# Kernel tuning notes

Hardware: AMD Instinct MI355X
Metric: run time of the kernel (lower is better)

Reference implementation:

```python
import jax, jax.numpy as jnp
import numpy as np

SEQ, D_IN, D_OUT = 8192, 1024, 1024

def setup_inputs() -> dict:
    key = jax.random.key(0)
    kx, kq, kk, kv = jax.random.split(key, 4)
    scale = 1.0 / np.sqrt(D_IN)
    return {
        "x": jax.random.normal(kx, (SEQ, D_IN), dtype=jnp.float32),
        "Wq": jax.random.normal(kq, (D_OUT, D_IN), dtype=jnp.float32) * scale,
        "Wk": jax.random.normal(kk, (D_OUT, D_IN), dtype=jnp.float32) * scale,
        "Wv": jax.random.normal(kv, (D_OUT, D_IN), dtype=jnp.float32) * scale,
    }

def reference(x, Wq, Wk, Wv):
    # nn.Linear: y = x @ W.T (no bias)
    q = x @ Wq.T            # [S, d_out]
    k = x @ Wk.T            # [S, d_out]
    v = x @ Wv.T            # [S, d_out]
    d_k = k.shape[-1]
    scores = (q @ k.T) / jnp.sqrt(jnp.float32(d_k))   # [S, S]
    attn = jax.nn.softmax(scores, axis=-1)
    return attn @ v         # [S, d_out]
```

## Files before the change

### kernel.cpp

```cpp
#include <hip/hip_runtime.h>

typedef unsigned short ushort_t;
typedef __attribute__((ext_vector_type(8))) __bf16 bf16x8;
typedef __attribute__((ext_vector_type(8))) unsigned short ushort8;
typedef __attribute__((ext_vector_type(4))) float f32x4;

#define SEQ 8192
#define DIN 1024
#define DOUT 1024

#define OM_BF16 0
#define OM_F32  1
#define OM_EXP  2
#define OM_NORM 3

__device__ __forceinline__ ushort_t f2bf(float f) {
  union { float f; unsigned u; } c; c.f = f;
  unsigned u = c.u;
  return (ushort_t)((u + 0x7fffu + ((u >> 16) & 1u)) >> 16);
}

__device__ __forceinline__ void async16(ushort_t* lds, const ushort_t* g) {
  __builtin_amdgcn_global_load_lds(
      (__attribute__((address_space(1))) void*)g,
      (__attribute__((address_space(3))) void*)lds, 16, 0, 0);
}

__global__ __launch_bounds__(256) void cvt_all_kernel(
    const float* __restrict__ x, const float* __restrict__ wq,
    const float* __restrict__ wk, const float* __restrict__ wv,
    ushort_t* __restrict__ xb, ushort_t* __restrict__ wqkb,
    ushort_t* __restrict__ wvb) {
  int b = blockIdx.x;
  const float* src;
  ushort_t* dst;
  int idx;
  if (b < 8192) {
    src = x; dst = xb; idx = b * 256 + threadIdx.x;
  } else {
    int r = b - 8192;
    int w = r >> 10;
    idx = (r & 1023) * 256 + threadIdx.x;
    if (w == 0)      { src = wq; dst = wqkb; }
    else if (w == 1) { src = wk; dst = wqkb + DOUT * DIN; }
    else             { src = wv; dst = wvb; }
  }
  float4 f = ((const float4*)src)[idx];
  ushort4 o;
  o.x = f2bf(f.x); o.y = f2bf(f.y); o.z = f2bf(f.z); o.w = f2bf(f.w);
  ((ushort4*)dst)[idx] = o;
}

template <int OUTMODE, int SWZ, int BK>
__global__ __launch_bounds__(256) void gemm_bt(const ushort_t* __restrict__ A,
                                               const ushort_t* __restrict__ B,
                                               void* __restrict__ C,
                                               int lda, int ldb, int ldc,
                                               int K, float scale,
                                               float* __restrict__ rsp, int nparts) {
  constexpr int CPR = BK / 8;
  __shared__ ushort_t As[128 * BK];
  __shared__ ushort_t Bs[128 * BK];
  const int t = threadIdx.x;
  const int lane = t & 63;
  const int wave = t >> 6;
  const int wr = wave >> 1, wc = wave & 1;
  const int quad = lane >> 4, r16 = lane & 15;

  int mt, nt;
  if (SWZ == 1) {
    mt = blockIdx.x * (gridDim.y >> 3) + (blockIdx.y >> 3);
    nt = blockIdx.y & 7;
  } else {
    mt = blockIdx.y;
    nt = blockIdx.x;
  }
  const int rowBase = mt * 128;
  const int colBase = nt * 128;

  f32x4 acc[4][4] = {};

  const int nk = K / BK;
  for (int kt = 0; kt < nk; ++kt) {
    #pragma unroll
    for (int i = 0; i < BK / 16; ++i) {
      int c = t + i * 256;
      int row = c / CPR;
      int kq = c & (CPR - 1);
      int kqs = (kq & ~7) | ((kq & 7) ^ (row & 7));
      async16(&As[c * 8], A + (size_t)(rowBase + row) * lda + kt * BK + kqs * 8);
      async16(&Bs[c * 8], B + (size_t)(colBase + row) * ldb + kt * BK + kqs * 8);
    }
    __syncthreads();
    #pragma unroll
    for (int ks = 0; ks < BK / 32; ++ks) {
      bf16x8 af[4], bfr[4];
      #pragma unroll
      for (int mi = 0; mi < 4; ++mi) {
        int row = wr * 64 + mi * 16 + r16;
        int kq = ks * 4 + quad;
        int c = row * CPR + ((kq & ~7) | ((kq & 7) ^ (row & 7)));
        af[mi] = *(const bf16x8*)&As[c * 8];
      }
      #pragma unroll
      for (int ni = 0; ni < 4; ++ni) {
        int row = wc * 64 + ni * 16 + r16;
        int kq = ks * 4 + quad;
        int c = row * CPR + ((kq & ~7) | ((kq & 7) ^ (row & 7)));
        bfr[ni] = *(const bf16x8*)&Bs[c * 8];
      }
      #pragma unroll
      for (int mi = 0; mi < 4; ++mi)
        #pragma unroll
        for (int ni = 0; ni < 4; ++ni)
          acc[mi][ni] = __builtin_amdgcn_mfma_f32_16x16x32_bf16(af[mi], bfr[ni],
                                                                acc[mi][ni], 0, 0, 0);
    }
    __syncthreads();
  }

  float iv[4][4];
  if (OUTMODE == OM_NORM) {
    float* invs = (float*)As;
    if (t < 128) {
      float s = 0.f;
      for (int p2 = 0; p2 < nparts; ++p2)
        s += rsp[(size_t)p2 * SEQ + rowBase + t];
      invs[t] = 1.0f / s;
    }
    __syncthreads();
    #pragma unroll
    for (int mi = 0; mi < 4; ++mi)
      #pragma unroll
      for (int r = 0; r < 4; ++r)
        iv[mi][r] = invs[wr * 64 + mi * 16 + quad * 4 + r];
  }

  float psum[4][4];
  if (OUTMODE == OM_EXP) {
    #pragma unroll
    for (int mi = 0; mi < 4; ++mi)
      #pragma unroll
      for (int r = 0; r < 4; ++r) psum[mi][r] = 0.f;
  }

  #pragma unroll
  for (int mi = 0; mi < 4; ++mi)
    #pragma unroll
    for (int ni = 0; ni < 4; ++ni)
      #pragma unroll
      for (int r = 0; r < 4; ++r) {
        int grow = rowBase + wr * 64 + mi * 16 + quad * 4 + r;
        int gcol = colBase + wc * 64 + ni * 16 + r16;
        float a = acc[mi][ni][r];
        if (OUTMODE == OM_F32) {
          ((float*)C)[(size_t)grow * ldc + gcol] = a * scale;
        } else if (OUTMODE == OM_BF16) {
          ((ushort_t*)C)[(size_t)grow * ldc + gcol] = f2bf(a * scale);
        } else if (OUTMODE == OM_EXP) {
          float e = __expf(a * scale);
          psum[mi][r] += e;
          ((ushort_t*)C)[(size_t)grow * ldc + gcol] = f2bf(e);
        } else {
          ((float*)C)[(size_t)grow * ldc + gcol] = a * iv[mi][r];
        }
      }

  if (OUTMODE == OM_EXP) {
    float* lds_rs = (float*)As;
    #pragma unroll
    for (int mi = 0; mi < 4; ++mi)
      #pragma unroll
      for (int r = 0; r < 4; ++r) {
        float s = psum[mi][r];
        s += __shfl_xor(s, 1, 64);
        s += __shfl_xor(s, 2, 64);
        s += __shfl_xor(s, 4, 64);
        s += __shfl_xor(s, 8, 64);
        if (r16 == 0)
          lds_rs[wc * 128 + wr * 64 + mi * 16 + quad * 4 + r] = s;
      }
    __syncthreads();
    if (t < 128)
      rsp[(size_t)nt * SEQ + rowBase + t] = lds_rs[t] + lds_rs[128 + t];
  }
}

extern "C" void kernel_launch(void* const* d_in, const int* in_sizes, int n_in,
                              void* d_out, int out_size, void* d_ws, size_t ws_size,
                              hipStream_t stream) {
  const float* x  = (const float*)d_in[0];
  const float* Wq = (const float*)d_in[1];
  const float* Wk = (const float*)d_in[2];
  const float* Wv = (const float*)d_in[3];
  float* out = (float*)d_out;

  char* p = (char*)d_ws;
  ushort_t* xb   = (ushort_t*)p; p += (size_t)SEQ * DIN * 2;
  ushort_t* wqkb = (ushort_t*)p; p += (size_t)2 * DOUT * DIN * 2;
  ushort_t* wvb  = (ushort_t*)p; p += (size_t)DOUT * DIN * 2;
  ushort_t* qkb  = (ushort_t*)p; p += (size_t)SEQ * 2 * DOUT * 2;
  ushort_t* vtb  = (ushort_t*)p; p += (size_t)DOUT * SEQ * 2;
  float*    rsp  = (float*)p;    p += (size_t)64 * SEQ * 4;
  ushort_t* Sb   = (ushort_t*)p; p += (size_t)SEQ * SEQ * 2;

  cvt_all_kernel<<<8192 + 3 * 1024, 256, 0, stream>>>(x, Wq, Wk, Wv, xb, wqkb, wvb);

  dim3 blk(256);
  gemm_bt<OM_BF16, 0, 64><<<dim3(2048 / 128, SEQ / 128), blk, 0, stream>>>(
      xb, wqkb, qkb, DIN, DIN, 2 * DOUT, DIN, 1.0f, nullptr, 0);

  gemm_bt<OM_BF16, 0, 128><<<dim3(SEQ / 128, DOUT / 128), blk, 0, stream>>>(
      wvb, xb, vtb, DIN, DIN, SEQ, DIN, 1.0f, nullptr, 0);

  gemm_bt<OM_EXP, 0, 64><<<dim3(SEQ / 128, SEQ / 128), blk, 0, stream>>>(
      qkb, qkb + DOUT, Sb, 2 * DOUT, 2 * DOUT, SEQ, DIN, 0.03125f, rsp, 64);

  gemm_bt<OM_NORM, 1, 128><<<dim3(DOUT / 128, SEQ / 128), blk, 0, stream>>>(
      Sb, vtb, out, SEQ, SEQ, DOUT, SEQ, 1.0f, rsp, 64);
}
```

Measured before the change: 478.2 us.

## Store LDS tiles in MFMA-fragment order, precompute row-sum inverses, use exp2

Reorganizes the shared-memory tile layout so each 16-row by 32-k panel is stored in exactly the order the MFMA lanes read it. This removes per-iteration XOR swizzle index arithmetic and gives contiguous conflict-free fragment loads, with global pointers precomputed once and advanced by BK each step. The per-block reduction of 64 partial row sums in the final GEMM is moved into a small separate kernel that writes inverse sums once. The exponential now uses exp2 with log2(e) folded into the scale. The new global load pattern reads 16-byte pieces across 16 rows per panel, which may coalesce less well than the previous row-contiguous pattern.

Result: slower. 761.1 us (+59.2%).

```diff
diff --git a/kernel.cpp b/kernel.cpp
--- a/kernel.cpp
+++ b/kernel.cpp
@@ -2,7 +2,6 @@
 
 typedef unsigned short ushort_t;
 typedef __attribute__((ext_vector_type(8))) __bf16 bf16x8;
-typedef __attribute__((ext_vector_type(8))) unsigned short ushort8;
 typedef __attribute__((ext_vector_type(4))) float f32x4;
 
 #define SEQ 8192
@@ -51,14 +50,24 @@
   ((ushort4*)dst)[idx] = o;
 }
 
+__global__ __launch_bounds__(256) void rowsum_inv_kernel(const float* __restrict__ rsp,
+                                                         float* __restrict__ invrs) {
+  int r = blockIdx.x * 256 + threadIdx.x;
+  float s = 0.f;
+  #pragma unroll
+  for (int p2 = 0; p2 < 64; ++p2) s += rsp[p2 * SEQ + r];
+  invrs[r] = 1.0f / s;
+}
+
 template <int OUTMODE, int SWZ, int BK>
 __global__ __launch_bounds__(256) void gemm_bt(const ushort_t* __restrict__ A,
                                                const ushort_t* __restrict__ B,
                                                void* __restrict__ C,
                                                int lda, int ldb, int ldc,
                                                int K, float scale,
-                                               float* __restrict__ rsp, int nparts) {
-  constexpr int CPR = BK / 8;
+                                               float* __restrict__ rsp,
+                                               const float* __restrict__ invrs) {
+  constexpr int NI = BK / 16;
   __shared__ ushort_t As[128 * BK];
   __shared__ ushort_t Bs[128 * BK];
   const int t = threadIdx.x;
@@ -78,37 +87,39 @@
   const int rowBase = mt * 128;
   const int colBase = nt * 128;
 
+  const ushort_t* gA[NI];
+  const ushort_t* gB[NI];
+  #pragma unroll
+  for (int i = 0; i < NI; ++i) {
+    int s = t + i * 256;
+    int ks = s >> 9;
+    int pnl = (s >> 6) & 7;
+    int l = s & 63;
+    int row = pnl * 16 + (l & 15);
+    int kk = ks * 32 + ((l >> 4) & 3) * 8;
+    gA[i] = A + (size_t)(rowBase + row) * lda + kk;
+    gB[i] = B + (size_t)(colBase + row) * ldb + kk;
+  }
+
   f32x4 acc[4][4] = {};
 
   const int nk = K / BK;
   for (int kt = 0; kt < nk; ++kt) {
     #pragma unroll
-    for (int i = 0; i < BK / 16; ++i) {
-      int c = t + i * 256;
-      int row = c / CPR;
-      int kq = c & (CPR - 1);
-      int kqs = (kq & ~7) | ((kq & 7) ^ (row & 7));
-      async16(&As[c * 8], A + (size_t)(rowBase + row) * lda + kt * BK + kqs * 8);
-      async16(&Bs[c * 8], B + (size_t)(colBase + row) * ldb + kt * BK + kqs * 8);
+    for (int i = 0; i < NI; ++i) {
+      async16(&As[(t + i * 256) * 8], gA[i]); gA[i] += BK;
+      async16(&Bs[(t + i * 256) * 8], gB[i]); gB[i] += BK;
     }
     __syncthreads();
     #pragma unroll
     for (int ks = 0; ks < BK / 32; ++ks) {
       bf16x8 af[4], bfr[4];
       #pragma unroll
-      for (int mi = 0; mi < 4; ++mi) {
-        int row = wr * 64 + mi * 16 + r16;
-        int kq = ks * 4 + quad;
-        int c = row * CPR + ((kq & ~7) | ((kq & 7) ^ (row & 7)));
-        af[mi] = *(const bf16x8*)&As[c * 8];
-      }
-      #pragma unroll
-      for (int ni = 0; ni < 4; ++ni) {
-        int row = wc * 64 + ni * 16 + r16;
-        int kq = ks * 4 + quad;
-        int c = row * CPR + ((kq & ~7) | ((kq & 7) ^ (row & 7)));
-        bfr[ni] = *(const bf16x8*)&Bs[c * 8];
-      }
+      for (int mi = 0; mi < 4; ++mi)
+        af[mi] = *(const bf16x8*)&As[((ks * 8 + wr * 4 + mi) << 9) + lane * 8];
+      #pragma unroll
+      for (int ni = 0; ni < 4; ++ni)
+        bfr[ni] = *(const bf16x8*)&Bs[((ks * 8 + wc * 4 + ni) << 9) + lane * 8];
       #pragma unroll
       for (int mi = 0; mi < 4; ++mi)
         #pragma unroll
@@ -121,19 +132,11 @@
 
   float iv[4][4];
   if (OUTMODE == OM_NORM) {
-    float* invs = (float*)As;
-    if (t < 128) {
-      float s = 0.f;
-      for (int p2 = 0; p2 < nparts; ++p2)
-        s += rsp[(size_t)p2 * SEQ + rowBase + t];
-      invs[t] = 1.0f / s;
-    }
-    __syncthreads();
     #pragma unroll
     for (int mi = 0; mi < 4; ++mi)
       #pragma unroll
       for (int r = 0; r < 4; ++r)
-        iv[mi][r] = invs[wr * 64 + mi * 16 + quad * 4 + r];
+        iv[mi][r] = invrs[rowBase + wr * 64 + mi * 16 + quad * 4 + r];
   }
 
   float psum[4][4];
@@ -158,7 +161,7 @@
         } else if (OUTMODE == OM_BF16) {
           ((ushort_t*)C)[(size_t)grow * ldc + gcol] = f2bf(a * scale);
         } else if (OUTMODE == OM_EXP) {
-          float e = __expf(a * scale);
+          float e = exp2f(a * scale);
           psum[mi][r] += e;
           ((ushort_t*)C)[(size_t)grow * ldc + gcol] = f2bf(e);
         } else {
@@ -202,20 +205,24 @@
   ushort_t* qkb  = (ushort_t*)p; p += (size_t)SEQ * 2 * DOUT * 2;
   ushort_t* vtb  = (ushort_t*)p; p += (size_t)DOUT * SEQ * 2;
   float*    rsp  = (float*)p;    p += (size_t)64 * SEQ * 4;
+  float*    irs  = (float*)p;    p += (size_t)SEQ * 4;
   ushort_t* Sb   = (ushort_t*)p; p += (size_t)SEQ * SEQ * 2;
 
   cvt_all_kernel<<<8192 + 3 * 1024, 256, 0, stream>>>(x, Wq, Wk, Wv, xb, wqkb, wvb);
 
   dim3 blk(256);
   gemm_bt<OM_BF16, 0, 64><<<dim3(2048 / 128, SEQ / 128), blk, 0, stream>>>(
-      xb, wqkb, qkb, DIN, DIN, 2 * DOUT, DIN, 1.0f, nullptr, 0);
+      xb, wqkb, qkb, DIN, DIN, 2 * DOUT, DIN, 1.0f, nullptr, nullptr);
 
   gemm_bt<OM_BF16, 0, 128><<<dim3(SEQ / 128, DOUT / 128), blk, 0, stream>>>(
-      wvb, xb, vtb, DIN, DIN, SEQ, DIN, 1.0f, nullptr, 0);
+      wvb, xb, vtb, DIN, DIN, SEQ, DIN, 1.0f, nullptr, nullptr);
 
   gemm_bt<OM_EXP, 0, 64><<<dim3(SEQ / 128, SEQ / 128), blk, 0, stream>>>(
-      qkb, qkb + DOUT, Sb, 2 * DOUT, 2 * DOUT, SEQ, DIN, 0.03125f, rsp, 64);
+      qkb, qkb + DOUT, Sb, 2 * DOUT, 2 * DOUT, SEQ, DIN,
+      0.03125f * 1.44269504f, rsp, nullptr);
+
+  rowsum_inv_kernel<<<SEQ / 256, blk, 0, stream>>>(rsp, irs);
 
   gemm_bt<OM_NORM, 1, 128><<<dim3(DOUT / 128, SEQ / 128), blk, 0, stream>>>(
-      Sb, vtb, out, SEQ, SEQ, DOUT, SEQ, 1.0f, rsp, 64);
-}
+      Sb, vtb, out, SEQ, SEQ, DOUT, SEQ, 1.0f, nullptr, irs);
+}
```
